# Performance work log

Measured on AMD Instinct MI355X. Metric: run time of the kernel, lower is better.

## Reference

```python
import jax, jax.numpy as jnp
import numpy as np

V = 50000      # vocab_size
E = 300        # EMBED_SIZE
H = 128        # HIDDEN_SIZE // NUM_DIRS
T = 12         # num_tags
SOS = 3
EOS = 4
NEG = -10000.0


def setup_inputs() -> dict:
    key = jax.random.key(0)
    ks = jax.random.split(key, 14)
    B, S = 128, 512
    x = jax.random.randint(ks[0], (B, S), 0, V)
    y0 = jax.random.randint(ks[1], (B, S), 0, T)
    s = 1.0 / np.sqrt(H)
    u = lambda k, shape: jax.random.uniform(k, shape, jnp.float32, -s, s)
    embed = jax.random.normal(ks[2], (V, E), jnp.float32)
    # torch LSTM gate layout: [i, f, g, o] stacked along first dim (4H)
    Wih_f = u(ks[3], (4 * H, E)); Whh_f = u(ks[4], (4 * H, H)); b_f = u(ks[5], (4 * H,)) + u(ks[6], (4 * H,))
    Wih_b = u(ks[7], (4 * H, E)); Whh_b = u(ks[8], (4 * H, H)); b_b = u(ks[9], (4 * H,)) + u(ks[10], (4 * H,))
    Wout = u(ks[11], (T, 2 * H)); bout = u(ks[12], (T,))
    trans = jax.random.normal(ks[13], (T, T), jnp.float32)
    trans = trans.at[SOS, :].set(NEG).at[:, EOS].set(NEG)
    return dict(x=x, y0=y0, embed=embed,
                Wih_f=Wih_f, Whh_f=Whh_f, b_f=b_f,
                Wih_b=Wih_b, Whh_b=Whh_b, b_b=b_b,
                Wout=Wout, bout=bout, trans=trans)


def _lstm_dir(emb, Wih, Whh, b):
    # emb: [B, S, E] -> hidden states [B, S, H] for one direction
    B = emb.shape[0]
    def step(carry, x_t):
        h, c = carry
        g = x_t @ Wih.T + h @ Whh.T + b  # [B, 4H]
        i, f, gg, o = jnp.split(g, 4, axis=-1)
        c = jax.nn.sigmoid(f) * c + jax.nn.sigmoid(i) * jnp.tanh(gg)
        h = jax.nn.sigmoid(o) * jnp.tanh(c)
        return (h, c), h
    init = (jnp.zeros((B, H), emb.dtype), jnp.zeros((B, H), emb.dtype))
    _, hs = jax.lax.scan(step, init, jnp.swapaxes(emb, 0, 1))  # hs: [S, B, H]
    return jnp.swapaxes(hs, 0, 1)


def reference(x, y0, embed, Wih_f, Whh_f, b_f, Wih_b, Whh_b, b_b, Wout, bout, trans):
    # ---- lstm: embed -> biLSTM -> linear, emissions y: [B, S, T]
    emb = embed[x]
    hf = _lstm_dir(emb, Wih_f, Whh_f, b_f)
    hb = _lstm_dir(emb[:, ::-1], Wih_b, Whh_b, b_b)[:, ::-1]
    y = jnp.concatenate([hf, hb], axis=-1) @ Wout.T + bout

    B = x.shape[0]
    # ---- CRF partition Z via forward algorithm (trans[i, j] = score j -> i)
    score0 = jnp.full((B, T), NEG, y.dtype).at[:, SOS].set(0.0)
    def step(score, emit_t):
        new = jax.nn.logsumexp(score[:, None, :] + trans[None, :, :], axis=-1) + emit_t
        return new, None
    scoreZ, _ = jax.lax.scan(step, score0, jnp.swapaxes(y, 0, 1))
    Z = jax.nn.logsumexp(scoreZ + trans[EOS][None, :], axis=-1)  # [B]

    # ---- gold path score (vectorized version of crf.score)
    y0p = jnp.concatenate([jnp.full((B, 1), SOS, y0.dtype), y0], axis=1)  # [B, S+1]
    emit = jnp.take_along_axis(y, y0p[:, 1:, None], axis=2)[..., 0].sum(axis=1)
    tr = trans[y0p[:, 1:], y0p[:, :-1]].sum(axis=1)
    gold = emit + tr + trans[EOS, y0p[:, -1]]

    return Z - gold  # [B] negative log-likelihood per example
```

## Files before the change

### kernel.cpp

```cpp
#include <hip/hip_runtime.h>

typedef unsigned short u16;
typedef __attribute__((ext_vector_type(8))) short short8;
typedef __attribute__((ext_vector_type(4))) float floatx4;

#define SOS 3
#define EOS 4
#define NEGV -10000.0f
#define LOG2E 1.442695041f
#define TWOLOG2E 2.885390082f

__device__ __forceinline__ u16 f2bf(float f) {
  union { float f; unsigned int i; } v; v.f = f;
  unsigned int r = (v.i + 0x7FFFu + ((v.i >> 16) & 1u)) >> 16;
  return (u16)r;
}
__device__ __forceinline__ void gload_lds16(const u16* g, u16* l) {
  __builtin_amdgcn_global_load_lds((const __attribute__((address_space(1))) void*)g,
                                   (__attribute__((address_space(3))) void*)l, 16, 0, 0);
}

__global__ __launch_bounds__(256) void gather_kernel(const float* __restrict__ embed,
                                                     const int* __restrict__ x,
                                                     u16* __restrict__ A) {
  int idx = blockIdx.x * 256 + threadIdx.x;
  int row = idx / 40;
  int c8 = idx - row * 40;
  int col0 = c8 * 8;
  int b = row & 127, t = row >> 7;
  const float* src = embed + (size_t)x[b * 512 + t] * 300 + col0;
  short8 o;
  if (col0 + 8 <= 300) {
    float4 f0 = *(const float4*)(src);
    float4 f1 = *(const float4*)(src + 4);
    o[0] = (short)f2bf(f0.x); o[1] = (short)f2bf(f0.y);
    o[2] = (short)f2bf(f0.z); o[3] = (short)f2bf(f0.w);
    o[4] = (short)f2bf(f1.x); o[5] = (short)f2bf(f1.y);
    o[6] = (short)f2bf(f1.z); o[7] = (short)f2bf(f1.w);
  } else {
    #pragma unroll
    for (int e = 0; e < 8; ++e)
      o[e] = (col0 + e < 300) ? (short)f2bf(src[e]) : (short)0;
  }
  *(short8*)&A[(size_t)row * 320 + col0] = o;
}

__global__ __launch_bounds__(256) void wpack_kernel(const float* __restrict__ Wf,
                                                    const float* __restrict__ Wb,
                                                    u16* __restrict__ Wp) {
  int idx = blockIdx.x * 256 + threadIdx.x;
  int p = idx / 40;
  int c8 = idx - p * 40;
  int col0 = c8 * 8;
  int dd = p >> 9, q = p & 511;
  int j = q >> 2, g = q & 3;
  const float* src = (dd ? Wb : Wf) + (size_t)(g * 128 + j) * 300;
  short8 o;
  #pragma unroll
  for (int e = 0; e < 8; ++e)
    o[e] = (col0 + e < 300) ? (short)f2bf(src[col0 + e]) : (short)0;
  *(short8*)&Wp[(size_t)p * 320 + col0] = o;
}

__global__ __launch_bounds__(256) void gemm_kernel(const u16* __restrict__ A,
                                                   const u16* __restrict__ B,
                                                   const float* __restrict__ bf_,
                                                   const float* __restrict__ bb_,
                                                   u16* __restrict__ G) {
  __shared__ u16 At[2][128 * 32];
  __shared__ u16 Bt[2][128 * 32];
  const int n = blockIdx.x;
  const int xcd = n & 7, rr = n >> 3;
  const int bx = xcd * 64 + (rr >> 3);
  const int by = rr & 7;
  const int tid = threadIdx.x;
  const int lane = tid & 63;
  const int wave = tid >> 6;
  const int wr = wave >> 1, wc = wave & 1;
  const int arow0 = bx * 128;
  const int bcol0 = by * 128;
  floatx4 acc[4][4] = {};
  const int fq = lane >> 4;
  const int fr = lane & 15;
  const int sr = wave * 32 + (lane >> 2);
  const int sc = (lane & 3) * 8;

#define STAGE(BUF_, K0_) { \
    gload_lds16(&A[(size_t)(arow0 + sr) * 320 + (K0_) + sc],      &At[BUF_][wave * 1024]); \
    gload_lds16(&A[(size_t)(arow0 + sr + 16) * 320 + (K0_) + sc], &At[BUF_][wave * 1024 + 512]); \
    gload_lds16(&B[(size_t)(bcol0 + sr) * 320 + (K0_) + sc],      &Bt[BUF_][wave * 1024]); \
    gload_lds16(&B[(size_t)(bcol0 + sr + 16) * 320 + (K0_) + sc], &Bt[BUF_][wave * 1024 + 512]); \
  }

  STAGE(0, 0);
  __builtin_amdgcn_sched_barrier(0);
  asm volatile("s_waitcnt vmcnt(0)" ::: "memory");
  __builtin_amdgcn_sched_barrier(0);
  __builtin_amdgcn_s_barrier();
  __builtin_amdgcn_sched_barrier(0);

  int cur = 0;
  #pragma unroll 1
  for (int ks = 0; ks < 10; ++ks) {
    if (ks < 9) STAGE(cur ^ 1, (ks + 1) * 32);
    short8 af[4], bfr[4];
    #pragma unroll
    for (int mi = 0; mi < 4; ++mi)
      af[mi] = *(const short8*)&At[cur][(wr * 64 + mi * 16 + fr) * 32 + fq * 8];
    #pragma unroll
    for (int ni = 0; ni < 4; ++ni)
      bfr[ni] = *(const short8*)&Bt[cur][(wc * 64 + ni * 16 + fr) * 32 + fq * 8];
    #pragma unroll
    for (int mi = 0; mi < 4; ++mi)
      #pragma unroll
      for (int ni = 0; ni < 4; ++ni)
        acc[mi][ni] = __builtin_amdgcn_mfma_f32_16x16x32_bf16(bfr[ni], af[mi], acc[mi][ni], 0, 0, 0);
    __builtin_amdgcn_sched_barrier(0);
    asm volatile("s_waitcnt vmcnt(0)" ::: "memory");
    __builtin_amdgcn_sched_barrier(0);
    __builtin_amdgcn_s_barrier();
    __builtin_amdgcn_sched_barrier(0);
    cur ^= 1;
  }
#undef STAGE

  #pragma unroll
  for (int ni = 0; ni < 4; ++ni) {
    const int colq = bcol0 + wc * 64 + ni * 16 + fq * 4;
    const int jj = (colq & 511) >> 2;
    const float* bsrc = (colq >= 512) ? bb_ : bf_;
    const float b0 = bsrc[jj], b1 = bsrc[128 + jj], b2 = bsrc[256 + jj], b3 = bsrc[384 + jj];
    #pragma unroll
    for (int mi = 0; mi < 4; ++mi) {
      const int row = arow0 + wr * 64 + mi * 16 + fr;
      unsigned q0 = f2bf(acc[mi][ni][0] + b0);
      unsigned q1 = f2bf(acc[mi][ni][1] + b1);
      unsigned q2 = f2bf(acc[mi][ni][2] + b2);
      unsigned q3 = f2bf(acc[mi][ni][3] + b3);
      uint2 pk;
      pk.x = q0 | (q1 << 16);
      pk.y = q2 | (q3 << 16);
      *(uint2*)&G[(size_t)row * 1024 + colq] = pk;
    }
  }
}

__global__ __launch_bounds__(512, 2) void lstm_fused_kernel(const u16* __restrict__ Gp,
                                                            const float* __restrict__ Whh_f,
                                                            const float* __restrict__ Whh_b,
                                                            u16* __restrict__ hs) {
  const int bid = blockIdx.x;
  const int d  = bid >> 5;
  const int b0 = (bid & 31) * 4;
  const int tid = threadIdx.x;
  const int w = tid >> 6, lane = tid & 63;
  const int fr = lane & 15, fq = lane >> 4;
  const float* Wd = d ? Whh_b : Whh_f;

  short8 Wfr[4][4];
  #pragma unroll
  for (int tt = 0; tt < 4; ++tt) {
    const int orow = (fr & 3) * 128 + (16 * w + 4 * tt + (fr >> 2));
    #pragma unroll
    for (int kk = 0; kk < 4; ++kk) {
      const float* src = Wd + (size_t)orow * 128 + fq * 8 + kk * 32;
      float4 x0 = *(const float4*)src;
      float4 x1 = *(const float4*)(src + 4);
      short8 o;
      o[0] = (short)f2bf(x0.x); o[1] = (short)f2bf(x0.y);
      o[2] = (short)f2bf(x0.z); o[3] = (short)f2bf(x0.w);
      o[4] = (short)f2bf(x1.x); o[5] = (short)f2bf(x1.y);
      o[6] = (short)f2bf(x1.z); o[7] = (short)f2bf(x1.w);
      Wfr[tt][kk] = o;
    }
  }

  __shared__ __align__(16) u16 hbuf[2][512];
  for (int i = tid; i < 1024; i += 512) (&hbuf[0][0])[i] = 0;
  __syncthreads();

  const int ts = d ? -1 : 1;
  const int t0 = d ? 511 : 0;
  const int bb  = fr & 3;
  const int ttl = fr >> 2;
  const int jj  = 16 * w + 4 * ttl + fq;

  const int ho0 = bb * 128 + (((fq      + 4 * bb) & 15) << 3);
  const int ho1 = bb * 128 + (((fq + 4  + 4 * bb) & 15) << 3);
  const int ho2 = bb * 128 + (((fq + 8  + 4 * bb) & 15) << 3);
  const int ho3 = bb * 128 + (((fq + 12 + 4 * bb) & 15) << 3);
  const int hwi = bb * 128 + ((((jj >> 3) + 4 * bb) & 15) << 3) + (jj & 7);

  const long long gstep = (long long)ts * 131072;
  const long long hstep = (long long)ts * 256;
  const u16* gld = Gp + (long long)t0 * 131072 + (b0 + bb) * 1024 + d * 512 + 4 * jj;
  u16* hsp = hs + (size_t)(b0 + bb) * 131072 + (long long)t0 * 256 + d * 128 + jj;
  float cst = 0.f;

  uint2 gA, gB, gC;
  gA = *(const uint2*)gld; gld += gstep;
  gB = *(const uint2*)gld; gld += gstep;
  gC = *(const uint2*)gld; gld += gstep;

  u16* hr = &hbuf[0][0];
  u16* hw = &hbuf[1][0];

#define STEPN(GR_, PF_) { \
    short8 f0 = *(const short8*)(hr + ho0); \
    short8 f1 = *(const short8*)(hr + ho1); \
    short8 f2 = *(const short8*)(hr + ho2); \
    short8 f3 = *(const short8*)(hr + ho3); \
    floatx4 a0 = {0.f, 0.f, 0.f, 0.f}; \
    floatx4 a1 = a0, a2 = a0, a3 = a0; \
    a0 = __builtin_amdgcn_mfma_f32_16x16x32_bf16(Wfr[0][0], f0, a0, 0, 0, 0); \
    a1 = __builtin_amdgcn_mfma_f32_16x16x32_bf16(Wfr[1][0], f0, a1, 0, 0, 0); \
    a2 = __builtin_amdgcn_mfma_f32_16x16x32_bf16(Wfr[2][0], f0, a2, 0, 0, 0); \
    a3 = __builtin_amdgcn_mfma_f32_16x16x32_bf16(Wfr[3][0], f0, a3, 0, 0, 0); \
    a0 = __builtin_amdgcn_mfma_f32_16x16x32_bf16(Wfr[0][1], f1, a0, 0, 0, 0); \
    a1 = __builtin_amdgcn_mfma_f32_16x16x32_bf16(Wfr[1][1], f1, a1, 0, 0, 0); \
    a2 = __builtin_amdgcn_mfma_f32_16x16x32_bf16(Wfr[2][1], f1, a2, 0, 0, 0); \
    a3 = __builtin_amdgcn_mfma_f32_16x16x32_bf16(Wfr[3][1], f1, a3, 0, 0, 0); \
    a0 = __builtin_amdgcn_mfma_f32_16x16x32_bf16(Wfr[0][2], f2, a0, 0, 0, 0); \
    a1 = __builtin_amdgcn_mfma_f32_16x16x32_bf16(Wfr[1][2], f2, a1, 0, 0, 0); \
    a2 = __builtin_amdgcn_mfma_f32_16x16x32_bf16(Wfr[2][2], f2, a2, 0, 0, 0); \
    a3 = __builtin_amdgcn_mfma_f32_16x16x32_bf16(Wfr[3][2], f2, a3, 0, 0, 0); \
    a0 = __builtin_amdgcn_mfma_f32_16x16x32_bf16(Wfr[0][3], f3, a0, 0, 0, 0); \
    a1 = __builtin_amdgcn_mfma_f32_16x16x32_bf16(Wfr[1][3], f3, a1, 0, 0, 0); \
    a2 = __builtin_amdgcn_mfma_f32_16x16x32_bf16(Wfr[2][3], f3, a2, 0, 0, 0); \
    a3 = __builtin_amdgcn_mfma_f32_16x16x32_bf16(Wfr[3][3], f3, a3, 0, 0, 0); \
    const bool s0 = (ttl & 1), s1 = (ttl & 2); \
    float p0 = s1 ? (s0 ? a3[0] : a2[0]) : (s0 ? a1[0] : a0[0]); \
    float p1 = s1 ? (s0 ? a3[1] : a2[1]) : (s0 ? a1[1] : a0[1]); \
    float p2 = s1 ? (s0 ? a3[2] : a2[2]) : (s0 ? a1[2] : a0[2]); \
    float p3 = s1 ? (s0 ? a3[3] : a2[3]) : (s0 ? a1[3] : a0[3]); \
    float G0 = __builtin_bit_cast(float, GR_.x << 16); \
    float G1 = __builtin_bit_cast(float, GR_.x & 0xffff0000u); \
    float G2 = __builtin_bit_cast(float, GR_.y << 16); \
    float G3 = __builtin_bit_cast(float, GR_.y & 0xffff0000u); \
    if (PF_) { GR_ = *(const uint2*)gld; gld += gstep; } \
    float i_ = p0 + G0, f_ = p1 + G1, g_ = p2 + G2, o_ = p3 + G3; \
    float p  = __builtin_amdgcn_exp2f(__builtin_amdgcn_fmed3f(g_ * TWOLOG2E, -40.f, 40.f)); \
    float qi = __builtin_amdgcn_exp2f(__builtin_amdgcn_fmed3f(i_ * -LOG2E, -40.f, 40.f)); \
    float qf = __builtin_amdgcn_exp2f(__builtin_amdgcn_fmed3f(f_ * -LOG2E, -40.f, 40.f)); \
    float qo = __builtin_amdgcn_exp2f(__builtin_amdgcn_fmed3f(o_ * -LOG2E, -40.f, 40.f)); \
    float D1 = (1.f + qi) * (p + 1.f); \
    float qf1 = 1.f + qf; \
    float cn = (cst * D1 + (p - 1.f) * qf1) * __builtin_amdgcn_rcpf(qf1 * D1); \
    cst = cn; \
    float v = __builtin_amdgcn_exp2f(__builtin_amdgcn_fmed3f(cn * TWOLOG2E, -40.f, 40.f)); \
    float h = (v - 1.f) * __builtin_amdgcn_rcpf((1.f + qo) * (v + 1.f)); \
    u16 hb = f2bf(h); \
    hw[hwi] = hb; \
    *hsp = hb; \
    hsp += hstep; \
    __builtin_amdgcn_sched_barrier(0); \
    asm volatile("s_waitcnt lgkmcnt(0)"); \
    __builtin_amdgcn_sched_barrier(0); \
    __builtin_amdgcn_s_barrier(); \
    __builtin_amdgcn_sched_barrier(0); \
    u16* tp_ = hr; hr = hw; hw = tp_; \
  }

  #pragma unroll 1
  for (int it = 0; it < 170; ++it) {
    STEPN(gA, true);
    STEPN(gB, true);
    STEPN(gC, true);
  }
  STEPN(gA, false);
  STEPN(gB, false);
#undef STEPN
}

__global__ __launch_bounds__(256) void emis_kernel(const u16* __restrict__ hs,
                                                   const float* __restrict__ Wout,
                                                   const float* __restrict__ bout,
                                                   float* __restrict__ y) {
  __shared__ float Ws[12 * 256];
  __shared__ float bs[12];
  const int tid = threadIdx.x;
  for (int i = tid; i < 12 * 256; i += 256) Ws[i] = Wout[i];
  if (tid < 12) bs[tid] = bout[tid];
  __syncthreads();
  const int wave = tid >> 6, lane = tid & 63;
  const size_t m = (size_t)blockIdx.x * 4 + wave;
  uint2 hv = *(const uint2*)&hs[m * 256 + lane * 4];
  float h0 = __builtin_bit_cast(float, hv.x << 16);
  float h1 = __builtin_bit_cast(float, hv.x & 0xffff0000u);
  float h2 = __builtin_bit_cast(float, hv.y << 16);
  float h3 = __builtin_bit_cast(float, hv.y & 0xffff0000u);
  float p[12];
  #pragma unroll
  for (int tg = 0; tg < 12; ++tg) {
    const float* wv = &Ws[tg * 256 + lane * 4];
    p[tg] = h0 * wv[0] + h1 * wv[1] + h2 * wv[2] + h3 * wv[3];
  }
  #pragma unroll
  for (int off = 32; off; off >>= 1)
    #pragma unroll
    for (int tg = 0; tg < 12; ++tg)
      p[tg] += __shfl_xor(p[tg], off);
  if (lane == 0) {
    #pragma unroll
    for (int tg = 0; tg < 12; ++tg)
      y[m * 12 + tg] = p[tg] + bs[tg];
  }
}

__global__ __launch_bounds__(64) void crf_kernel(const float* __restrict__ y,
                                                 const int* __restrict__ y0,
                                                 const float* __restrict__ trans,
                                                 float* __restrict__ out) {
  const int b = blockIdx.x;
  const int lane = threadIdx.x;
  __shared__ float trs[144];
  for (int i = lane; i < 144; i += 64) trs[i] = trans[i];
  __syncthreads();
  const int row = (lane < 12) ? lane : 0;
  float etr[12];
  #pragma unroll
  for (int j = 0; j < 12; ++j) etr[j] = __expf(trs[row * 12 + j]);
  float etreos = (lane < 12) ? __expf(trs[EOS * 12 + lane]) : 0.f;
  float u = (lane == SOS) ? 1.f : 0.f;
  float base = 0.f;
  const float* yb = y + (size_t)b * 512 * 12;
  float pe0 = __expf(yb[row]);
  float pe1 = __expf(yb[12 + row]);
  for (int t = 0; t < 512; ++t) {
    float pe = pe0;
    pe0 = pe1;
    if (t + 2 < 512) pe1 = __expf(yb[(t + 2) * 12 + row]);
    float U[12];
    #pragma unroll
    for (int j = 0; j < 12; ++j)
      U[j] = __builtin_bit_cast(float, __builtin_amdgcn_readlane(__builtin_bit_cast(int, u), j));
    float m_[12];
    #pragma unroll
    for (int j = 0; j < 12; ++j) m_[j] = etr[j] * U[j];
    float d = (((m_[0] + m_[1]) + (m_[2] + m_[3])) + ((m_[4] + m_[5]) + (m_[6] + m_[7])))
            + ((m_[8] + m_[9]) + (m_[10] + m_[11]));
    float uraw = d * pe;
    float r = __builtin_bit_cast(float, __builtin_amdgcn_readlane(__builtin_bit_cast(int, uraw), 0));
    base += __logf(r);
    u = uraw * __builtin_amdgcn_rcpf(r);
  }
  float vv = (lane < 12) ? u * etreos : 0.f;
  #pragma unroll
  for (int off = 32; off; off >>= 1) vv += __shfl_xor(vv, off);
  const float Z = base + __logf(vv);
  const int* y0b = y0 + (size_t)b * 512;
  float acc = 0.f;
  for (int t = lane; t < 512; t += 64) {
    int cur = y0b[t];
    int prev = t ? y0b[t - 1] : SOS;
    acc += yb[t * 12 + cur] + trs[cur * 12 + prev];
  }
  #pragma unroll
  for (int off = 32; off; off >>= 1) acc += __shfl_xor(acc, off);
  if (lane == 0) {
    float gold = acc + trs[EOS * 12 + y0b[511]];
    out[b] = Z - gold;
  }
}

extern "C" void kernel_launch(void* const* d_in, const int* in_sizes, int n_in,
                              void* d_out, int out_size, void* d_ws, size_t ws_size,
                              hipStream_t stream) {
  (void)in_sizes; (void)n_in; (void)out_size; (void)ws_size;
  const int*   x     = (const int*)d_in[0];
  const int*   y0    = (const int*)d_in[1];
  const float* embed = (const float*)d_in[2];
  const float* Wih_f = (const float*)d_in[3];
  const float* Whh_f = (const float*)d_in[4];
  const float* b_f   = (const float*)d_in[5];
  const float* Wih_b = (const float*)d_in[6];
  const float* Whh_b = (const float*)d_in[7];
  const float* b_b   = (const float*)d_in[8];
  const float* Wout  = (const float*)d_in[9];
  const float* bout  = (const float*)d_in[10];
  const float* trans = (const float*)d_in[11];
  float* out = (float*)d_out;

  char* ws = (char*)d_ws;
  u16*   A  = (u16*)(ws);
  u16*   Wp = (u16*)(ws + 41943040);
  u16*   G  = (u16*)(ws + 42598400);
  u16*   hs = (u16*)(ws + 176816128);
  float* yy = (float*)(ws + 210370560);

  gather_kernel<<<10240, 256, 0, stream>>>(embed, x, A);
  wpack_kernel<<<160, 256, 0, stream>>>(Wih_f, Wih_b, Wp);
  gemm_kernel<<<4096, 256, 0, stream>>>(A, Wp, b_f, b_b, G);
  lstm_fused_kernel<<<64, 512, 0, stream>>>(G, Whh_f, Whh_b, hs);
  emis_kernel<<<16384, 256, 0, stream>>>(hs, Wout, bout, yy);
  crf_kernel<<<128, 64, 0, stream>>>(yy, y0, trans, out);
}
```

Baseline: 555.9 us.

## Fuse embedding gather and weight packing into input-projection GEMM; batch emission rows

The separate gather and weight-pack kernels are removed. The GEMM now loads fp32 embedding rows and Wih rows directly from global memory into registers, converts them to bf16 with packed convert instructions, and writes them to a single LDS buffer, prefetching the next K slice into registers. This drops the bf16 intermediate write and read plus two launches, but the GEMM re-reads fp32 data redundantly across tiles and gives up the async global-to-LDS double buffering. The emission kernel also processes four row groups per block, using a quarter as many blocks to amortise its LDS weight load.

```diff
diff --git a/kernel.cpp b/kernel.cpp
--- a/kernel.cpp
+++ b/kernel.cpp
@@ -15,60 +15,26 @@
   unsigned int r = (v.i + 0x7FFFu + ((v.i >> 16) & 1u)) >> 16;
   return (u16)r;
 }
-__device__ __forceinline__ void gload_lds16(const u16* g, u16* l) {
-  __builtin_amdgcn_global_load_lds((const __attribute__((address_space(1))) void*)g,
-                                   (__attribute__((address_space(3))) void*)l, 16, 0, 0);
-}
-
-__global__ __launch_bounds__(256) void gather_kernel(const float* __restrict__ embed,
-                                                     const int* __restrict__ x,
-                                                     u16* __restrict__ A) {
-  int idx = blockIdx.x * 256 + threadIdx.x;
-  int row = idx / 40;
-  int c8 = idx - row * 40;
-  int col0 = c8 * 8;
-  int b = row & 127, t = row >> 7;
-  const float* src = embed + (size_t)x[b * 512 + t] * 300 + col0;
-  short8 o;
-  if (col0 + 8 <= 300) {
-    float4 f0 = *(const float4*)(src);
-    float4 f1 = *(const float4*)(src + 4);
-    o[0] = (short)f2bf(f0.x); o[1] = (short)f2bf(f0.y);
-    o[2] = (short)f2bf(f0.z); o[3] = (short)f2bf(f0.w);
-    o[4] = (short)f2bf(f1.x); o[5] = (short)f2bf(f1.y);
-    o[6] = (short)f2bf(f1.z); o[7] = (short)f2bf(f1.w);
-  } else {
-    #pragma unroll
-    for (int e = 0; e < 8; ++e)
-      o[e] = (col0 + e < 300) ? (short)f2bf(src[e]) : (short)0;
-  }
-  *(short8*)&A[(size_t)row * 320 + col0] = o;
-}
-
-__global__ __launch_bounds__(256) void wpack_kernel(const float* __restrict__ Wf,
-                                                    const float* __restrict__ Wb,
-                                                    u16* __restrict__ Wp) {
-  int idx = blockIdx.x * 256 + threadIdx.x;
-  int p = idx / 40;
-  int c8 = idx - p * 40;
-  int col0 = c8 * 8;
-  int dd = p >> 9, q = p & 511;
-  int j = q >> 2, g = q & 3;
-  const float* src = (dd ? Wb : Wf) + (size_t)(g * 128 + j) * 300;
-  short8 o;
-  #pragma unroll
-  for (int e = 0; e < 8; ++e)
-    o[e] = (col0 + e < 300) ? (short)f2bf(src[col0 + e]) : (short)0;
-  *(short8*)&Wp[(size_t)p * 320 + col0] = o;
-}
-
-__global__ __launch_bounds__(256) void gemm_kernel(const u16* __restrict__ A,
-                                                   const u16* __restrict__ B,
+__device__ __forceinline__ short8 pack8(float4 a, float4 b) {
+  unsigned p0, p1, p2, p3;
+  asm("v_cvt_pk_bf16_f32 %0, %1, %2" : "=v"(p0) : "v"(a.x), "v"(a.y));
+  asm("v_cvt_pk_bf16_f32 %0, %1, %2" : "=v"(p1) : "v"(a.z), "v"(a.w));
+  asm("v_cvt_pk_bf16_f32 %0, %1, %2" : "=v"(p2) : "v"(b.x), "v"(b.y));
+  asm("v_cvt_pk_bf16_f32 %0, %1, %2" : "=v"(p3) : "v"(b.z), "v"(b.w));
+  union { unsigned u[4]; short8 s; } r;
+  r.u[0] = p0; r.u[1] = p1; r.u[2] = p2; r.u[3] = p3;
+  return r.s;
+}
+
+__global__ __launch_bounds__(256) void gemm_kernel(const float* __restrict__ embed,
+                                                   const int* __restrict__ x,
+                                                   const float* __restrict__ Wf,
+                                                   const float* __restrict__ Wb,
                                                    const float* __restrict__ bf_,
                                                    const float* __restrict__ bb_,
                                                    u16* __restrict__ G) {
-  __shared__ u16 At[2][128 * 32];
-  __shared__ u16 Bt[2][128 * 32];
+  __shared__ u16 At[128 * 32];
+  __shared__ u16 Bt[128 * 32];
   const int n = blockIdx.x;
   const int xcd = n & 7, rr = n >> 3;
   const int bx = xcd * 64 + (rr >> 3);
@@ -82,47 +48,67 @@
   floatx4 acc[4][4] = {};
   const int fq = lane >> 4;
   const int fr = lane & 15;
-  const int sr = wave * 32 + (lane >> 2);
   const int sc = (lane & 3) * 8;
-
-#define STAGE(BUF_, K0_) { \
-    gload_lds16(&A[(size_t)(arow0 + sr) * 320 + (K0_) + sc],      &At[BUF_][wave * 1024]); \
-    gload_lds16(&A[(size_t)(arow0 + sr + 16) * 320 + (K0_) + sc], &At[BUF_][wave * 1024 + 512]); \
-    gload_lds16(&B[(size_t)(bcol0 + sr) * 320 + (K0_) + sc],      &Bt[BUF_][wave * 1024]); \
-    gload_lds16(&B[(size_t)(bcol0 + sr + 16) * 320 + (K0_) + sc], &Bt[BUF_][wave * 1024 + 512]); \
-  }
-
-  STAGE(0, 0);
-  __builtin_amdgcn_sched_barrier(0);
-  asm volatile("s_waitcnt vmcnt(0)" ::: "memory");
-  __builtin_amdgcn_sched_barrier(0);
-  __builtin_amdgcn_s_barrier();
-  __builtin_amdgcn_sched_barrier(0);
-
-  int cur = 0;
+  const int srow = wave * 32 + (lane >> 2);
+
+  const int m0 = arow0 + srow,      m1 = arow0 + srow + 16;
+  const float* ea0 = embed + (size_t)x[(m0 & 127) * 512 + (m0 >> 7)] * 300;
+  const float* ea1 = embed + (size_t)x[(m1 & 127) * 512 + (m1 >> 7)] * 300;
+  const int p0 = bcol0 + srow,      p1 = bcol0 + srow + 16;
+  const float* eb0 = ((p0 >> 9) ? Wb : Wf) + (size_t)(((p0 & 511) & 3) * 128 + ((p0 & 511) >> 2)) * 300;
+  const float* eb1 = ((p1 >> 9) ? Wb : Wf) + (size_t)(((p1 & 511) & 3) * 128 + ((p1 & 511) >> 2)) * 300;
+  u16* da0 = &At[wave * 1024 + lane * 8];
+  u16* da1 = da0 + 512;
+  u16* db0 = &Bt[wave * 1024 + lane * 8];
+  u16* db1 = db0 + 512;
+
+  float4 ra0, ra1, rb0, rb1, ra0b, ra1b, rb0b, rb1b;
+#define LOADR(K0_) { \
+    ra0  = *(const float4*)(ea0 + (K0_) + sc); ra0b = *(const float4*)(ea0 + (K0_) + sc + 4); \
+    ra1  = *(const float4*)(ea1 + (K0_) + sc); ra1b = *(const float4*)(ea1 + (K0_) + sc + 4); \
+    rb0  = *(const float4*)(eb0 + (K0_) + sc); rb0b = *(const float4*)(eb0 + (K0_) + sc + 4); \
+    rb1  = *(const float4*)(eb1 + (K0_) + sc); rb1b = *(const float4*)(eb1 + (K0_) + sc + 4); \
+  }
+#define LOADR_TAIL() {  \
+    float t_[8]; \
+    _Pragma("unroll") for (int e = 0; e < 8; ++e) { int c_ = 288 + sc + e; t_[e] = (c_ < 300) ? ea0[c_] : 0.f; } \
+    ra0 = make_float4(t_[0], t_[1], t_[2], t_[3]); ra0b = make_float4(t_[4], t_[5], t_[6], t_[7]); \
+    _Pragma("unroll") for (int e = 0; e < 8; ++e) { int c_ = 288 + sc + e; t_[e] = (c_ < 300) ? ea1[c_] : 0.f; } \
+    ra1 = make_float4(t_[0], t_[1], t_[2], t_[3]); ra1b = make_float4(t_[4], t_[5], t_[6], t_[7]); \
+    _Pragma("unroll") for (int e = 0; e < 8; ++e) { int c_ = 288 + sc + e; t_[e] = (c_ < 300) ? eb0[c_] : 0.f; } \
+    rb0 = make_float4(t_[0], t_[1], t_[2], t_[3]); rb0b = make_float4(t_[4], t_[5], t_[6], t_[7]); \
+    _Pragma("unroll") for (int e = 0; e < 8; ++e) { int c_ = 288 + sc + e; t_[e] = (c_ < 300) ? eb1[c_] : 0.f; } \
+    rb1 = make_float4(t_[0], t_[1], t_[2], t_[3]); rb1b = make_float4(t_[4], t_[5], t_[6], t_[7]); \
+  }
+
+  LOADR(0);
   #pragma unroll 1
   for (int ks = 0; ks < 10; ++ks) {
-    if (ks < 9) STAGE(cur ^ 1, (ks + 1) * 32);
+    *(short8*)da0 = pack8(ra0, ra0b);
+    *(short8*)da1 = pack8(ra1, ra1b);
+    *(short8*)db0 = pack8(rb0, rb0b);
+    *(short8*)db1 = pack8(rb1, rb1b);
+    __syncthreads();
+    if (ks < 9) {
+      if (ks == 8) { LOADR_TAIL(); }
+      else         { LOADR((ks + 1) * 32); }
+    }
     short8 af[4], bfr[4];
     #pragma unroll
     for (int mi = 0; mi < 4; ++mi)
-      af[mi] = *(const short8*)&At[cur][(wr * 64 + mi * 16 + fr) * 32 + fq * 8];
+      af[mi] = *(const short8*)&At[(wr * 64 + mi * 16 + fr) * 32 + fq * 8];
     #pragma unroll
     for (int ni = 0; ni < 4; ++ni)
-      bfr[ni] = *(const short8*)&Bt[cur][(wc * 64 + ni * 16 + fr) * 32 + fq * 8];
+      bfr[ni] = *(const short8*)&Bt[(wc * 64 + ni * 16 + fr) * 32 + fq * 8];
     #pragma unroll
     for (int mi = 0; mi < 4; ++mi)
       #pragma unroll
       for (int ni = 0; ni < 4; ++ni)
         acc[mi][ni] = __builtin_amdgcn_mfma_f32_16x16x32_bf16(bfr[ni], af[mi], acc[mi][ni], 0, 0, 0);
-    __builtin_amdgcn_sched_barrier(0);
-    asm volatile("s_waitcnt vmcnt(0)" ::: "memory");
-    __builtin_amdgcn_sched_barrier(0);
-    __builtin_amdgcn_s_barrier();
-    __builtin_amdgcn_sched_barrier(0);
-    cur ^= 1;
-  }
-#undef STAGE
+    __syncthreads();
+  }
+#undef LOADR
+#undef LOADR_TAIL
 
   #pragma unroll
   for (int ni = 0; ni < 4; ++ni) {
@@ -283,27 +269,30 @@
   if (tid < 12) bs[tid] = bout[tid];
   __syncthreads();
   const int wave = tid >> 6, lane = tid & 63;
-  const size_t m = (size_t)blockIdx.x * 4 + wave;
-  uint2 hv = *(const uint2*)&hs[m * 256 + lane * 4];
-  float h0 = __builtin_bit_cast(float, hv.x << 16);
-  float h1 = __builtin_bit_cast(float, hv.x & 0xffff0000u);
-  float h2 = __builtin_bit_cast(float, hv.y << 16);
-  float h3 = __builtin_bit_cast(float, hv.y & 0xffff0000u);
-  float p[12];
-  #pragma unroll
-  for (int tg = 0; tg < 12; ++tg) {
-    const float* wv = &Ws[tg * 256 + lane * 4];
-    p[tg] = h0 * wv[0] + h1 * wv[1] + h2 * wv[2] + h3 * wv[3];
-  }
-  #pragma unroll
-  for (int off = 32; off; off >>= 1)
-    #pragma unroll
-    for (int tg = 0; tg < 12; ++tg)
-      p[tg] += __shfl_xor(p[tg], off);
-  if (lane == 0) {
-    #pragma unroll
-    for (int tg = 0; tg < 12; ++tg)
-      y[m * 12 + tg] = p[tg] + bs[tg];
+  #pragma unroll
+  for (int it = 0; it < 4; ++it) {
+    const size_t m = ((size_t)blockIdx.x * 4 + it) * 4 + wave;
+    uint2 hv = *(const uint2*)&hs[m * 256 + lane * 4];
+    float h0 = __builtin_bit_cast(float, hv.x << 16);
+    float h1 = __builtin_bit_cast(float, hv.x & 0xffff0000u);
+    float h2 = __builtin_bit_cast(float, hv.y << 16);
+    float h3 = __builtin_bit_cast(float, hv.y & 0xffff0000u);
+    float p[12];
+    #pragma unroll
+    for (int tg = 0; tg < 12; ++tg) {
+      const float* wv = &Ws[tg * 256 + lane * 4];
+      p[tg] = h0 * wv[0] + h1 * wv[1] + h2 * wv[2] + h3 * wv[3];
+    }
+    #pragma unroll
+    for (int off = 32; off; off >>= 1)
+      #pragma unroll
+      for (int tg = 0; tg < 12; ++tg)
+        p[tg] += __shfl_xor(p[tg], off);
+    if (lane == 0) {
+      #pragma unroll
+      for (int tg = 0; tg < 12; ++tg)
+        y[m * 12 + tg] = p[tg] + bs[tg];
+    }
   }
 }
 
@@ -382,16 +371,12 @@
   float* out = (float*)d_out;
 
   char* ws = (char*)d_ws;
-  u16*   A  = (u16*)(ws);
-  u16*   Wp = (u16*)(ws + 41943040);
   u16*   G  = (u16*)(ws + 42598400);
   u16*   hs = (u16*)(ws + 176816128);
   float* yy = (float*)(ws + 210370560);
 
-  gather_kernel<<<10240, 256, 0, stream>>>(embed, x, A);
-  wpack_kernel<<<160, 256, 0, stream>>>(Wih_f, Wih_b, Wp);
-  gemm_kernel<<<4096, 256, 0, stream>>>(A, Wp, b_f, b_b, G);
+  gemm_kernel<<<4096, 256, 0, stream>>>(embed, x, Wih_f, Wih_b, b_f, b_b, G);
   lstm_fused_kernel<<<64, 512, 0, stream>>>(G, Whh_f, Whh_b, hs);
-  emis_kernel<<<16384, 256, 0, stream>>>(hs, Wout, bout, yy);
+  emis_kernel<<<4096, 256, 0, stream>>>(hs, Wout, bout, yy);
   crf_kernel<<<128, 64, 0, stream>>>(yy, y0, trans, out);
 }
```

Result: slower. 572.2 us (+2.9%).

## Fuse embedding gather into input GEMM and batch emission rows per block

Applied to the files above, without the earlier changes.

The separate gather kernel and its bf16 staging buffer A are removed. Each GEMM block now gathers its 128 embedding rows straight into a padded LDS tile, converts them with packed bf16 conversion instructions, and keeps that A panel resident while looping over all 8 N tiles. This avoids writing and re-reading A through global memory and drops one launch. The cost is far fewer GEMM blocks (512 instead of 4096), a large LDS footprint that lowers occupancy, and a non-pipelined first B stage for each N tile. The emission kernel also handles four row groups per block to cut the block count.

```diff
diff --git a/kernel.cpp b/kernel.cpp
--- a/kernel.cpp
+++ b/kernel.cpp
@@ -15,34 +15,19 @@
   unsigned int r = (v.i + 0x7FFFu + ((v.i >> 16) & 1u)) >> 16;
   return (u16)r;
 }
+__device__ __forceinline__ short8 pack8(float4 a, float4 b) {
+  unsigned p0, p1, p2, p3;
+  asm("v_cvt_pk_bf16_f32 %0, %1, %2" : "=v"(p0) : "v"(a.x), "v"(a.y));
+  asm("v_cvt_pk_bf16_f32 %0, %1, %2" : "=v"(p1) : "v"(a.z), "v"(a.w));
+  asm("v_cvt_pk_bf16_f32 %0, %1, %2" : "=v"(p2) : "v"(b.x), "v"(b.y));
+  asm("v_cvt_pk_bf16_f32 %0, %1, %2" : "=v"(p3) : "v"(b.z), "v"(b.w));
+  union { unsigned u[4]; short8 s; } r;
+  r.u[0] = p0; r.u[1] = p1; r.u[2] = p2; r.u[3] = p3;
+  return r.s;
+}
 __device__ __forceinline__ void gload_lds16(const u16* g, u16* l) {
   __builtin_amdgcn_global_load_lds((const __attribute__((address_space(1))) void*)g,
                                    (__attribute__((address_space(3))) void*)l, 16, 0, 0);
-}
-
-__global__ __launch_bounds__(256) void gather_kernel(const float* __restrict__ embed,
-                                                     const int* __restrict__ x,
-                                                     u16* __restrict__ A) {
-  int idx = blockIdx.x * 256 + threadIdx.x;
-  int row = idx / 40;
-  int c8 = idx - row * 40;
-  int col0 = c8 * 8;
-  int b = row & 127, t = row >> 7;
-  const float* src = embed + (size_t)x[b * 512 + t] * 300 + col0;
-  short8 o;
-  if (col0 + 8 <= 300) {
-    float4 f0 = *(const float4*)(src);
-    float4 f1 = *(const float4*)(src + 4);
-    o[0] = (short)f2bf(f0.x); o[1] = (short)f2bf(f0.y);
-    o[2] = (short)f2bf(f0.z); o[3] = (short)f2bf(f0.w);
-    o[4] = (short)f2bf(f1.x); o[5] = (short)f2bf(f1.y);
-    o[6] = (short)f2bf(f1.z); o[7] = (short)f2bf(f1.w);
-  } else {
-    #pragma unroll
-    for (int e = 0; e < 8; ++e)
-      o[e] = (col0 + e < 300) ? (short)f2bf(src[e]) : (short)0;
-  }
-  *(short8*)&A[(size_t)row * 320 + col0] = o;
 }
 
 __global__ __launch_bounds__(256) void wpack_kernel(const float* __restrict__ Wf,
@@ -62,85 +47,105 @@
   *(short8*)&Wp[(size_t)p * 320 + col0] = o;
 }
 
-__global__ __launch_bounds__(256) void gemm_kernel(const u16* __restrict__ A,
+__global__ __launch_bounds__(256) void gemm_kernel(const float* __restrict__ embed,
+                                                   const int* __restrict__ x,
                                                    const u16* __restrict__ B,
                                                    const float* __restrict__ bf_,
                                                    const float* __restrict__ bb_,
                                                    u16* __restrict__ G) {
-  __shared__ u16 At[2][128 * 32];
-  __shared__ u16 Bt[2][128 * 32];
-  const int n = blockIdx.x;
-  const int xcd = n & 7, rr = n >> 3;
-  const int bx = xcd * 64 + (rr >> 3);
-  const int by = rr & 7;
+  __shared__ __align__(16) u16 At[128 * 328];
+  __shared__ __align__(16) u16 Bt[2][128 * 32];
   const int tid = threadIdx.x;
   const int lane = tid & 63;
   const int wave = tid >> 6;
   const int wr = wave >> 1, wc = wave & 1;
-  const int arow0 = bx * 128;
-  const int bcol0 = by * 128;
-  floatx4 acc[4][4] = {};
+  const int arow0 = blockIdx.x * 128;
   const int fq = lane >> 4;
   const int fr = lane & 15;
+
+  {
+    const int r = tid >> 1;
+    const int half = tid & 1;
+    const int m = arow0 + r;
+    const float* ea = embed + (size_t)x[(m & 127) * 512 + (m >> 7)] * 300;
+    u16* dst = &At[r * 328 + half * 160];
+    #pragma unroll
+    for (int c8 = 0; c8 < 20; ++c8) {
+      const int col0 = half * 160 + c8 * 8;
+      short8 o;
+      if (col0 + 8 <= 300) {
+        float4 f0 = *(const float4*)(ea + col0);
+        float4 f1 = *(const float4*)(ea + col0 + 4);
+        o = pack8(f0, f1);
+      } else {
+        #pragma unroll
+        for (int e = 0; e < 8; ++e)
+          o[e] = (col0 + e < 300) ? (short)f2bf(ea[col0 + e]) : (short)0;
+      }
+      *(short8*)(dst + c8 * 8) = o;
+    }
+  }
+  __syncthreads();
+
   const int sr = wave * 32 + (lane >> 2);
   const int sc = (lane & 3) * 8;
 
-#define STAGE(BUF_, K0_) { \
-    gload_lds16(&A[(size_t)(arow0 + sr) * 320 + (K0_) + sc],      &At[BUF_][wave * 1024]); \
-    gload_lds16(&A[(size_t)(arow0 + sr + 16) * 320 + (K0_) + sc], &At[BUF_][wave * 1024 + 512]); \
-    gload_lds16(&B[(size_t)(bcol0 + sr) * 320 + (K0_) + sc],      &Bt[BUF_][wave * 1024]); \
-    gload_lds16(&B[(size_t)(bcol0 + sr + 16) * 320 + (K0_) + sc], &Bt[BUF_][wave * 1024 + 512]); \
-  }
-
-  STAGE(0, 0);
-  __builtin_amdgcn_sched_barrier(0);
-  asm volatile("s_waitcnt vmcnt(0)" ::: "memory");
-  __builtin_amdgcn_sched_barrier(0);
-  __builtin_amdgcn_s_barrier();
-  __builtin_amdgcn_sched_barrier(0);
-
-  int cur = 0;
   #pragma unroll 1
-  for (int ks = 0; ks < 10; ++ks) {
-    if (ks < 9) STAGE(cur ^ 1, (ks + 1) * 32);
-    short8 af[4], bfr[4];
-    #pragma unroll
-    for (int mi = 0; mi < 4; ++mi)
-      af[mi] = *(const short8*)&At[cur][(wr * 64 + mi * 16 + fr) * 32 + fq * 8];
-    #pragma unroll
-    for (int ni = 0; ni < 4; ++ni)
-      bfr[ni] = *(const short8*)&Bt[cur][(wc * 64 + ni * 16 + fr) * 32 + fq * 8];
-    #pragma unroll
-    for (int mi = 0; mi < 4; ++mi)
-      #pragma unroll
-      for (int ni = 0; ni < 4; ++ni)
-        acc[mi][ni] = __builtin_amdgcn_mfma_f32_16x16x32_bf16(bfr[ni], af[mi], acc[mi][ni], 0, 0, 0);
+  for (int by = 0; by < 8; ++by) {
+    const int bcol0 = by * 128;
+    floatx4 acc[4][4] = {};
+    gload_lds16(&B[(size_t)(bcol0 + sr) * 320 + sc],      &Bt[0][wave * 1024]);
+    gload_lds16(&B[(size_t)(bcol0 + sr + 16) * 320 + sc], &Bt[0][wave * 1024 + 512]);
     __builtin_amdgcn_sched_barrier(0);
     asm volatile("s_waitcnt vmcnt(0)" ::: "memory");
     __builtin_amdgcn_sched_barrier(0);
     __builtin_amdgcn_s_barrier();
     __builtin_amdgcn_sched_barrier(0);
-    cur ^= 1;
-  }
-#undef STAGE
-
-  #pragma unroll
-  for (int ni = 0; ni < 4; ++ni) {
-    const int colq = bcol0 + wc * 64 + ni * 16 + fq * 4;
-    const int jj = (colq & 511) >> 2;
-    const float* bsrc = (colq >= 512) ? bb_ : bf_;
-    const float b0 = bsrc[jj], b1 = bsrc[128 + jj], b2 = bsrc[256 + jj], b3 = bsrc[384 + jj];
-    #pragma unroll
-    for (int mi = 0; mi < 4; ++mi) {
-      const int row = arow0 + wr * 64 + mi * 16 + fr;
-      unsigned q0 = f2bf(acc[mi][ni][0] + b0);
-      unsigned q1 = f2bf(acc[mi][ni][1] + b1);
-      unsigned q2 = f2bf(acc[mi][ni][2] + b2);
-      unsigned q3 = f2bf(acc[mi][ni][3] + b3);
-      uint2 pk;
-      pk.x = q0 | (q1 << 16);
-      pk.y = q2 | (q3 << 16);
-      *(uint2*)&G[(size_t)row * 1024 + colq] = pk;
+    int cur = 0;
+    #pragma unroll 1
+    for (int ks = 0; ks < 10; ++ks) {
+      if (ks < 9) {
+        const int k1 = (ks + 1) * 32;
+        gload_lds16(&B[(size_t)(bcol0 + sr) * 320 + k1 + sc],      &Bt[cur ^ 1][wave * 1024]);
+        gload_lds16(&B[(size_t)(bcol0 + sr + 16) * 320 + k1 + sc], &Bt[cur ^ 1][wave * 1024 + 512]);
+      }
+      short8 af[4], bfr[4];
+      #pragma unroll
+      for (int mi = 0; mi < 4; ++mi)
+        af[mi] = *(const short8*)&At[(wr * 64 + mi * 16 + fr) * 328 + ks * 32 + fq * 8];
+      #pragma unroll
+      for (int ni = 0; ni < 4; ++ni)
+        bfr[ni] = *(const short8*)&Bt[cur][(wc * 64 + ni * 16 + fr) * 32 + fq * 8];
+      #pragma unroll
+      for (int mi = 0; mi < 4; ++mi)
+        #pragma unroll
+        for (int ni = 0; ni < 4; ++ni)
+          acc[mi][ni] = __builtin_amdgcn_mfma_f32_16x16x32_bf16(bfr[ni], af[mi], acc[mi][ni], 0, 0, 0);
+      __builtin_amdgcn_sched_barrier(0);
+      asm volatile("s_waitcnt vmcnt(0) lgkmcnt(0)" ::: "memory");
+      __builtin_amdgcn_sched_barrier(0);
+      __builtin_amdgcn_s_barrier();
+      __builtin_amdgcn_sched_barrier(0);
+      cur ^= 1;
+    }
+    #pragma unroll
+    for (int ni = 0; ni < 4; ++ni) {
+      const int colq = bcol0 + wc * 64 + ni * 16 + fq * 4;
+      const int jj = (colq & 511) >> 2;
+      const float* bsrc = (colq >= 512) ? bb_ : bf_;
+      const float b0 = bsrc[jj], b1 = bsrc[128 + jj], b2 = bsrc[256 + jj], b3 = bsrc[384 + jj];
+      #pragma unroll
+      for (int mi = 0; mi < 4; ++mi) {
+        const int row = arow0 + wr * 64 + mi * 16 + fr;
+        unsigned q0 = f2bf(acc[mi][ni][0] + b0);
+        unsigned q1 = f2bf(acc[mi][ni][1] + b1);
+        unsigned q2 = f2bf(acc[mi][ni][2] + b2);
+        unsigned q3 = f2bf(acc[mi][ni][3] + b3);
+        uint2 pk;
+        pk.x = q0 | (q1 << 16);
+        pk.y = q2 | (q3 << 16);
+        *(uint2*)&G[(size_t)row * 1024 + colq] = pk;
+      }
     }
   }
 }
@@ -283,27 +288,30 @@
   if (tid < 12) bs[tid] = bout[tid];
   __syncthreads();
   const int wave = tid >> 6, lane = tid & 63;
-  const size_t m = (size_t)blockIdx.x * 4 + wave;
-  uint2 hv = *(const uint2*)&hs[m * 256 + lane * 4];
-  float h0 = __builtin_bit_cast(float, hv.x << 16);
-  float h1 = __builtin_bit_cast(float, hv.x & 0xffff0000u);
-  float h2 = __builtin_bit_cast(float, hv.y << 16);
-  float h3 = __builtin_bit_cast(float, hv.y & 0xffff0000u);
-  float p[12];
-  #pragma unroll
-  for (int tg = 0; tg < 12; ++tg) {
-    const float* wv = &Ws[tg * 256 + lane * 4];
-    p[tg] = h0 * wv[0] + h1 * wv[1] + h2 * wv[2] + h3 * wv[3];
-  }
-  #pragma unroll
-  for (int off = 32; off; off >>= 1)
-    #pragma unroll
-    for (int tg = 0; tg < 12; ++tg)
-      p[tg] += __shfl_xor(p[tg], off);
-  if (lane == 0) {
-    #pragma unroll
-    for (int tg = 0; tg < 12; ++tg)
-      y[m * 12 + tg] = p[tg] + bs[tg];
+  #pragma unroll
+  for (int it = 0; it < 4; ++it) {
+    const size_t m = ((size_t)blockIdx.x * 4 + it) * 4 + wave;
+    uint2 hv = *(const uint2*)&hs[m * 256 + lane * 4];
+    float h0 = __builtin_bit_cast(float, hv.x << 16);
+    float h1 = __builtin_bit_cast(float, hv.x & 0xffff0000u);
+    float h2 = __builtin_bit_cast(float, hv.y << 16);
+    float h3 = __builtin_bit_cast(float, hv.y & 0xffff0000u);
+    float p[12];
+    #pragma unroll
+    for (int tg = 0; tg < 12; ++tg) {
+      const float* wv = &Ws[tg * 256 + lane * 4];
+      p[tg] = h0 * wv[0] + h1 * wv[1] + h2 * wv[2] + h3 * wv[3];
+    }
+    #pragma unroll
+    for (int off = 32; off; off >>= 1)
+      #pragma unroll
+      for (int tg = 0; tg < 12; ++tg)
+        p[tg] += __shfl_xor(p[tg], off);
+    if (lane == 0) {
+      #pragma unroll
+      for (int tg = 0; tg < 12; ++tg)
+        y[m * 12 + tg] = p[tg] + bs[tg];
+    }
   }
 }
 
@@ -382,16 +390,14 @@
   float* out = (float*)d_out;
 
   char* ws = (char*)d_ws;
-  u16*   A  = (u16*)(ws);
   u16*   Wp = (u16*)(ws + 41943040);
   u16*   G  = (u16*)(ws + 42598400);
   u16*   hs = (u16*)(ws + 176816128);
   float* yy = (float*)(ws + 210370560);
 
-  gather_kernel<<<10240, 256, 0, stream>>>(embed, x, A);
   wpack_kernel<<<160, 256, 0, stream>>>(Wih_f, Wih_b, Wp);
-  gemm_kernel<<<4096, 256, 0, stream>>>(A, Wp, b_f, b_b, G);
+  gemm_kernel<<<512, 256, 0, stream>>>(embed, x, Wp, b_f, b_b, G);
   lstm_fused_kernel<<<64, 512, 0, stream>>>(G, Whh_f, Whh_b, hs);
-  emis_kernel<<<16384, 256, 0, stream>>>(hs, Wout, bout, yy);
+  emis_kernel<<<4096, 256, 0, stream>>>(hs, Wout, bout, yy);
   crf_kernel<<<128, 64, 0, stream>>>(yy, y0, trans, out);
 }
```

New measurement: 590.3 us. 1.06x slower.

## Fuse input-projection GEMM with LSTM recurrence using counter-based producer/consumer sync

Applied to the files above, without the earlier changes.

Merges the input-projection GEMM and the recurrent LSTM kernel into one launch. The first 64 blocks run the LSTM recurrence. The remaining blocks compute GEMM tiles one timestep at a time, ordered from both ends of the sequence, and bump per-8-timestep atomic counters. LSTM blocks spin on those counters before prefetching the gate inputs they need, so the serial recurrence can start before the whole GEMM finishes. In exchange, the GEMM path loses double buffering and leaves half its waves idle under the 512-thread block size. The spin-waits also add risk if the LSTM blocks get far ahead of the GEMM producers.

```diff
diff --git a/kernel.cpp b/kernel.cpp
--- a/kernel.cpp
+++ b/kernel.cpp
@@ -47,7 +47,9 @@
 
 __global__ __launch_bounds__(256) void wpack_kernel(const float* __restrict__ Wf,
                                                     const float* __restrict__ Wb,
-                                                    u16* __restrict__ Wp) {
+                                                    u16* __restrict__ Wp,
+                                                    unsigned* __restrict__ cnt) {
+  if (blockIdx.x == 0 && threadIdx.x < 64) cnt[threadIdx.x] = 0u;
   int idx = blockIdx.x * 256 + threadIdx.x;
   int p = idx / 40;
   int c8 = idx - p * 40;
@@ -62,99 +64,90 @@
   *(short8*)&Wp[(size_t)p * 320 + col0] = o;
 }
 
-__global__ __launch_bounds__(256) void gemm_kernel(const u16* __restrict__ A,
-                                                   const u16* __restrict__ B,
-                                                   const float* __restrict__ bf_,
-                                                   const float* __restrict__ bb_,
-                                                   u16* __restrict__ G) {
-  __shared__ u16 At[2][128 * 32];
-  __shared__ u16 Bt[2][128 * 32];
-  const int n = blockIdx.x;
-  const int xcd = n & 7, rr = n >> 3;
-  const int bx = xcd * 64 + (rr >> 3);
-  const int by = rr & 7;
+__global__ __launch_bounds__(512, 2) void fused_kernel(const u16* __restrict__ A,
+                                                       const u16* __restrict__ B,
+                                                       const float* __restrict__ bf_,
+                                                       const float* __restrict__ bb_,
+                                                       u16* __restrict__ G,
+                                                       const float* __restrict__ Whh_f,
+                                                       const float* __restrict__ Whh_b,
+                                                       u16* __restrict__ hs,
+                                                       unsigned* __restrict__ cnt) {
+  __shared__ u16 At[128 * 32];
+  __shared__ u16 Bt[128 * 32];
+  __shared__ __align__(16) u16 hbuf[2][512];
+  const int bid = blockIdx.x;
   const int tid = threadIdx.x;
-  const int lane = tid & 63;
-  const int wave = tid >> 6;
-  const int wr = wave >> 1, wc = wave & 1;
-  const int arow0 = bx * 128;
-  const int bcol0 = by * 128;
-  floatx4 acc[4][4] = {};
-  const int fq = lane >> 4;
-  const int fr = lane & 15;
-  const int sr = wave * 32 + (lane >> 2);
-  const int sc = (lane & 3) * 8;
-
-#define STAGE(BUF_, K0_) { \
-    gload_lds16(&A[(size_t)(arow0 + sr) * 320 + (K0_) + sc],      &At[BUF_][wave * 1024]); \
-    gload_lds16(&A[(size_t)(arow0 + sr + 16) * 320 + (K0_) + sc], &At[BUF_][wave * 1024 + 512]); \
-    gload_lds16(&B[(size_t)(bcol0 + sr) * 320 + (K0_) + sc],      &Bt[BUF_][wave * 1024]); \
-    gload_lds16(&B[(size_t)(bcol0 + sr + 16) * 320 + (K0_) + sc], &Bt[BUF_][wave * 1024 + 512]); \
-  }
-
-  STAGE(0, 0);
-  __builtin_amdgcn_sched_barrier(0);
-  asm volatile("s_waitcnt vmcnt(0)" ::: "memory");
-  __builtin_amdgcn_sched_barrier(0);
-  __builtin_amdgcn_s_barrier();
-  __builtin_amdgcn_sched_barrier(0);
-
-  int cur = 0;
-  #pragma unroll 1
-  for (int ks = 0; ks < 10; ++ks) {
-    if (ks < 9) STAGE(cur ^ 1, (ks + 1) * 32);
-    short8 af[4], bfr[4];
-    #pragma unroll
-    for (int mi = 0; mi < 4; ++mi)
-      af[mi] = *(const short8*)&At[cur][(wr * 64 + mi * 16 + fr) * 32 + fq * 8];
-    #pragma unroll
-    for (int ni = 0; ni < 4; ++ni)
-      bfr[ni] = *(const short8*)&Bt[cur][(wc * 64 + ni * 16 + fr) * 32 + fq * 8];
-    #pragma unroll
-    for (int mi = 0; mi < 4; ++mi)
+  const int wave = tid >> 6, lane = tid & 63;
+  const int fq = lane >> 4, fr = lane & 15;
+
+  if (bid >= 64) {
+    const int g = bid - 64;
+    const int pair = g >> 4, side = (g >> 3) & 1, by = g & 7;
+    const int tIdx = side ? (511 - pair) : pair;
+    const int arow0 = tIdx << 7;
+    const int bcol0 = by << 7;
+    const bool act = (wave < 4);
+    const int wr = (wave & 3) >> 1, wc = wave & 1;
+    const int sr = (wave & 3) * 32 + (lane >> 2);
+    const int sc = (lane & 3) * 8;
+    floatx4 acc[4][4] = {};
+    #pragma unroll 1
+    for (int ks = 0; ks < 10; ++ks) {
+      if (act) {
+        const int k0 = ks * 32;
+        gload_lds16(&A[(size_t)(arow0 + sr) * 320 + k0 + sc],      &At[(wave & 3) * 1024]);
+        gload_lds16(&A[(size_t)(arow0 + sr + 16) * 320 + k0 + sc], &At[(wave & 3) * 1024 + 512]);
+        gload_lds16(&B[(size_t)(bcol0 + sr) * 320 + k0 + sc],      &Bt[(wave & 3) * 1024]);
+        gload_lds16(&B[(size_t)(bcol0 + sr + 16) * 320 + k0 + sc], &Bt[(wave & 3) * 1024 + 512]);
+      }
+      __syncthreads();
+      if (act) {
+        short8 af[4], bfr[4];
+        #pragma unroll
+        for (int mi = 0; mi < 4; ++mi)
+          af[mi] = *(const short8*)&At[(wr * 64 + mi * 16 + fr) * 32 + fq * 8];
+        #pragma unroll
+        for (int ni = 0; ni < 4; ++ni)
+          bfr[ni] = *(const short8*)&Bt[(wc * 64 + ni * 16 + fr) * 32 + fq * 8];
+        #pragma unroll
+        for (int mi = 0; mi < 4; ++mi)
+          #pragma unroll
+          for (int ni = 0; ni < 4; ++ni)
+            acc[mi][ni] = __builtin_amdgcn_mfma_f32_16x16x32_bf16(bfr[ni], af[mi], acc[mi][ni], 0, 0, 0);
+      }
+      __syncthreads();
+    }
+    if (act) {
       #pragma unroll
-      for (int ni = 0; ni < 4; ++ni)
-        acc[mi][ni] = __builtin_amdgcn_mfma_f32_16x16x32_bf16(bfr[ni], af[mi], acc[mi][ni], 0, 0, 0);
-    __builtin_amdgcn_sched_barrier(0);
-    asm volatile("s_waitcnt vmcnt(0)" ::: "memory");
-    __builtin_amdgcn_sched_barrier(0);
-    __builtin_amdgcn_s_barrier();
-    __builtin_amdgcn_sched_barrier(0);
-    cur ^= 1;
-  }
-#undef STAGE
-
-  #pragma unroll
-  for (int ni = 0; ni < 4; ++ni) {
-    const int colq = bcol0 + wc * 64 + ni * 16 + fq * 4;
-    const int jj = (colq & 511) >> 2;
-    const float* bsrc = (colq >= 512) ? bb_ : bf_;
-    const float b0 = bsrc[jj], b1 = bsrc[128 + jj], b2 = bsrc[256 + jj], b3 = bsrc[384 + jj];
-    #pragma unroll
-    for (int mi = 0; mi < 4; ++mi) {
-      const int row = arow0 + wr * 64 + mi * 16 + fr;
-      unsigned q0 = f2bf(acc[mi][ni][0] + b0);
-      unsigned q1 = f2bf(acc[mi][ni][1] + b1);
-      unsigned q2 = f2bf(acc[mi][ni][2] + b2);
-      unsigned q3 = f2bf(acc[mi][ni][3] + b3);
-      uint2 pk;
-      pk.x = q0 | (q1 << 16);
-      pk.y = q2 | (q3 << 16);
-      *(uint2*)&G[(size_t)row * 1024 + colq] = pk;
+      for (int ni = 0; ni < 4; ++ni) {
+        const int colq = bcol0 + wc * 64 + ni * 16 + fq * 4;
+        const int jj = (colq & 511) >> 2;
+        const float* bsrc = (colq >= 512) ? bb_ : bf_;
+        const float b0 = bsrc[jj], b1 = bsrc[128 + jj], b2 = bsrc[256 + jj], b3 = bsrc[384 + jj];
+        #pragma unroll
+        for (int mi = 0; mi < 4; ++mi) {
+          const int row = arow0 + wr * 64 + mi * 16 + fr;
+          unsigned q0 = f2bf(acc[mi][ni][0] + b0);
+          unsigned q1 = f2bf(acc[mi][ni][1] + b1);
+          unsigned q2 = f2bf(acc[mi][ni][2] + b2);
+          unsigned q3 = f2bf(acc[mi][ni][3] + b3);
+          uint2 pk;
+          pk.x = q0 | (q1 << 16);
+          pk.y = q2 | (q3 << 16);
+          *(uint2*)&G[(size_t)row * 1024 + colq] = pk;
+        }
+      }
     }
-  }
-}
-
-__global__ __launch_bounds__(512, 2) void lstm_fused_kernel(const u16* __restrict__ Gp,
-                                                            const float* __restrict__ Whh_f,
-                                                            const float* __restrict__ Whh_b,
-                                                            u16* __restrict__ hs) {
-  const int bid = blockIdx.x;
+    __syncthreads();
+    if (tid == 0)
+      __hip_atomic_fetch_add(&cnt[tIdx >> 3], 1u, __ATOMIC_RELEASE, __HIP_MEMORY_SCOPE_AGENT);
+    return;
+  }
+
   const int d  = bid >> 5;
   const int b0 = (bid & 31) * 4;
-  const int tid = threadIdx.x;
-  const int w = tid >> 6, lane = tid & 63;
-  const int fr = lane & 15, fq = lane >> 4;
+  const int w = wave;
   const float* Wd = d ? Whh_b : Whh_f;
 
   short8 Wfr[4][4];
@@ -174,8 +167,6 @@
       Wfr[tt][kk] = o;
     }
   }
-
-  __shared__ __align__(16) u16 hbuf[2][512];
   for (int i = tid; i < 1024; i += 512) (&hbuf[0][0])[i] = 0;
   __syncthreads();
 
@@ -184,6 +175,7 @@
   const int bb  = fr & 3;
   const int ttl = fr >> 2;
   const int jj  = 16 * w + 4 * ttl + fq;
+  const int wtrig = d ? 7 : 0;
 
   const int ho0 = bb * 128 + (((fq      + 4 * bb) & 15) << 3);
   const int ho1 = bb * 128 + (((fq + 4  + 4 * bb) & 15) << 3);
@@ -193,9 +185,16 @@
 
   const long long gstep = (long long)ts * 131072;
   const long long hstep = (long long)ts * 256;
-  const u16* gld = Gp + (long long)t0 * 131072 + (b0 + bb) * 1024 + d * 512 + 4 * jj;
+  const u16* gld = G + (long long)t0 * 131072 + (b0 + bb) * 1024 + d * 512 + 4 * jj;
   u16* hsp = hs + (size_t)(b0 + bb) * 131072 + (long long)t0 * 256 + d * 128 + jj;
   float cst = 0.f;
+  int pfT = t0 + 3 * ts;
+
+  if (tid == 0) {
+    while (__hip_atomic_load(&cnt[d ? 63 : 0], __ATOMIC_ACQUIRE, __HIP_MEMORY_SCOPE_AGENT) < 64u)
+      __builtin_amdgcn_s_sleep(8);
+  }
+  __syncthreads();
 
   uint2 gA, gB, gC;
   gA = *(const uint2*)gld; gld += gstep;
@@ -206,6 +205,13 @@
   u16* hw = &hbuf[1][0];
 
 #define STEPN(GR_, PF_) { \
+    if (PF_ && ((unsigned)pfT < 512u) && ((pfT & 7) == wtrig)) { \
+      if (tid == 0) { \
+        while (__hip_atomic_load(&cnt[pfT >> 3], __ATOMIC_ACQUIRE, __HIP_MEMORY_SCOPE_AGENT) < 64u) \
+          __builtin_amdgcn_s_sleep(8); \
+      } \
+      __syncthreads(); \
+    } \
     short8 f0 = *(const short8*)(hr + ho0); \
     short8 f1 = *(const short8*)(hr + ho1); \
     short8 f2 = *(const short8*)(hr + ho2); \
@@ -237,7 +243,7 @@
     float G1 = __builtin_bit_cast(float, GR_.x & 0xffff0000u); \
     float G2 = __builtin_bit_cast(float, GR_.y << 16); \
     float G3 = __builtin_bit_cast(float, GR_.y & 0xffff0000u); \
-    if (PF_) { GR_ = *(const uint2*)gld; gld += gstep; } \
+    if (PF_) { GR_ = *(const uint2*)gld; gld += gstep; pfT += ts; } \
     float i_ = p0 + G0, f_ = p1 + G1, g_ = p2 + G2, o_ = p3 + G3; \
     float p  = __builtin_amdgcn_exp2f(__builtin_amdgcn_fmed3f(g_ * TWOLOG2E, -40.f, 40.f)); \
     float qi = __builtin_amdgcn_exp2f(__builtin_amdgcn_fmed3f(i_ * -LOG2E, -40.f, 40.f)); \
@@ -382,16 +388,16 @@
   float* out = (float*)d_out;
 
   char* ws = (char*)d_ws;
-  u16*   A  = (u16*)(ws);
-  u16*   Wp = (u16*)(ws + 41943040);
-  u16*   G  = (u16*)(ws + 42598400);
-  u16*   hs = (u16*)(ws + 176816128);
-  float* yy = (float*)(ws + 210370560);
+  u16*      A   = (u16*)(ws);
+  u16*      Wp  = (u16*)(ws + 41943040);
+  u16*      G   = (u16*)(ws + 42598400);
+  u16*      hs  = (u16*)(ws + 176816128);
+  float*    yy  = (float*)(ws + 210370560);
+  unsigned* cnt = (unsigned*)(ws + 213516288);
 
   gather_kernel<<<10240, 256, 0, stream>>>(embed, x, A);
-  wpack_kernel<<<160, 256, 0, stream>>>(Wih_f, Wih_b, Wp);
-  gemm_kernel<<<4096, 256, 0, stream>>>(A, Wp, b_f, b_b, G);
-  lstm_fused_kernel<<<64, 512, 0, stream>>>(G, Whh_f, Whh_b, hs);
+  wpack_kernel<<<160, 256, 0, stream>>>(Wih_f, Wih_b, Wp, cnt);
+  fused_kernel<<<4160, 512, 0, stream>>>(A, Wp, b_f, b_b, G, Whh_f, Whh_b, hs, cnt);
   emis_kernel<<<16384, 256, 0, stream>>>(hs, Wout, bout, yy);
   crf_kernel<<<128, 64, 0, stream>>>(yy, y0, trans, out);
 }
```

After: 795.6 us. 43.1% more time.
